# Kernel optimization log

Hardware: AMD Instinct MI355X
Metric: run time of the kernel (lower is better)

Reference implementation:

```python
import jax, jax.numpy as jnp
import numpy as np

B, OBS, H, A = 500000, 128, 64, 16


def setup_inputs() -> dict:
    key = jax.random.key(0)
    ks = jax.random.split(key, 10)
    return {
        "x": jax.random.normal(ks[0], (B, OBS), dtype=jnp.float32),
        "hidden_states": jax.random.normal(ks[1], (B, H), dtype=jnp.float32),
        "active_masks": jax.random.randint(ks[2], (B,), 0, 2, dtype=jnp.int32),
        "fc1_w": jax.random.normal(ks[3], (H, OBS), dtype=jnp.float32) * 0.05,
        "fc1_b": jnp.zeros((H,), dtype=jnp.float32),
        "w_ih": jax.random.normal(ks[4], (3 * H, H), dtype=jnp.float32) * 0.05,
        "w_hh": jax.random.normal(ks[5], (3 * H, H), dtype=jnp.float32) * 0.05,
        "b_ih": jnp.zeros((3 * H,), dtype=jnp.float32),
        "b_hh": jnp.zeros((3 * H,), dtype=jnp.float32),
        "fc2_w": jax.random.normal(ks[6], (A, H), dtype=jnp.float32) * 0.01,
        "fc2_b": jnp.zeros((A,), dtype=jnp.float32),
    }


def reference(x, hidden_states, active_masks, fc1_w, fc1_b, w_ih, w_hh, b_ih, b_hh, fc2_w, fc2_b):
    # fc1 + tanh: [B, H]
    a = jnp.tanh(x @ fc1_w.T + fc1_b)
    # GRUCell (torch convention): gates = [r, z, n]
    gi = a @ w_ih.T + b_ih                      # [B, 3H]
    gh = hidden_states @ w_hh.T + b_hh          # [B, 3H]
    i_r, i_z, i_n = jnp.split(gi, 3, axis=-1)
    h_r, h_z, h_n = jnp.split(gh, 3, axis=-1)
    r = jax.nn.sigmoid(i_r + h_r)
    z = jax.nn.sigmoid(i_z + h_z)
    n = jnp.tanh(i_n + r * h_n)
    h_upd = (1.0 - z) * n + z * hidden_states
    # Selective update: active agents get the GRU step, sleepers keep state.
    mask = (active_masks != 0)[:, None]          # [B, 1]
    new_hidden = jnp.where(mask, h_upd, hidden_states)
    logits = new_hidden @ fc2_w.T + fc2_b        # [B, A]
    return logits, new_hidden
```

## Files before the change

### kernel.cpp

```cpp
#include <hip/hip_runtime.h>


#define BB   500000
#define OBSN 128
#define HD   64
#define ADIM 16
#define NTIL (BB / 16)
#define GRID 512
#define GWAV (GRID * 8)

typedef __attribute__((ext_vector_type(8))) short short8;
typedef __attribute__((ext_vector_type(4))) float f32x4;

__device__ __forceinline__ unsigned short f2b(float f) {
  union { float f; unsigned u; } c; c.f = f;
  return (unsigned short)((c.u + 0x7fffu + ((c.u >> 16) & 1u)) >> 16);
}
__device__ __forceinline__ unsigned pk2(float a, float b) {
  return (unsigned)f2b(a) | ((unsigned)f2b(b) << 16);
}
__device__ __forceinline__ short8 cvt_frag(float4 a, float4 b) {
  union { short8 v; unsigned u[4]; } t;
  t.u[0] = pk2(a.x, a.y); t.u[1] = pk2(a.z, a.w);
  t.u[2] = pk2(b.x, b.y); t.u[3] = pk2(b.z, b.w);
  return t.v;
}
__device__ __forceinline__ float fsigmoid(float x) {
  return __builtin_amdgcn_rcpf(1.f + __builtin_amdgcn_exp2f(-1.44269504f * x));
}
__device__ __forceinline__ float ftanh(float x) {
  return 1.f - 2.f * __builtin_amdgcn_rcpf(1.f + __builtin_amdgcn_exp2f(2.88539008f * x));
}

__global__ void convert_weights(const float* __restrict__ fc1_w,
                                const float* __restrict__ w_ih,
                                const float* __restrict__ w_hh,
                                const float* __restrict__ fc2_w,
                                unsigned short* __restrict__ ws) {
  int i = blockIdx.x * 256 + threadIdx.x;
  if (i < 8192) {
    int n = i >> 7, k = (i & 127) ^ ((n & 7) << 3);
    ws[i] = f2b(fc1_w[n * 128 + k]);
  } else if (i < 24576) {
    int j = i - 8192, n = j >> 7, k = (j & 127) ^ ((n & 7) << 3);
    float v = (k < 64) ? w_ih[n * 64 + k] : w_hh[n * 64 + (k - 64)];
    ws[i] = f2b(v);
  } else if (i < 28672) {
    int j = i - 24576, n = j >> 6, k = (j & 63) ^ ((n & 7) << 3);
    ws[i] = f2b(w_ih[8192 + n * 64 + k]);
  } else if (i < 32768) {
    int j = i - 28672, n = j >> 6, k = (j & 63) ^ ((n & 7) << 3);
    ws[i] = f2b(w_hh[8192 + n * 64 + k]);
  } else if (i < 33792) {
    int j = i - 32768, n = j >> 6, k = (j & 63) ^ ((n & 7) << 3);
    ws[i] = f2b(fc2_w[n * 64 + k]);
  }
}

struct Batch {
  float4 x[8];
  float4 h[4];
  int4   am4;
};

#define LDS_FENCE() asm volatile("s_waitcnt lgkmcnt(0)" ::: "memory")

__global__ __launch_bounds__(512) void gru_actor_main(
    const float* __restrict__ x, const float* __restrict__ hs,
    const int* __restrict__ am,
    const float* __restrict__ fc1_b, const float* __restrict__ b_ih,
    const float* __restrict__ b_hh, const float* __restrict__ fc2_b,
    const unsigned short* __restrict__ wb, float* __restrict__ out) {
  __shared__ __align__(16) unsigned short lw[33792];
  __shared__ __align__(16) unsigned short sb_all[8][16 * 72];
  __shared__ __align__(16) float hf_all[8][16 * 68];

  const int tid = threadIdx.x;
#pragma unroll
  for (int i = 0; i < 9; ++i) {
    int c = tid + i * 512;
    if (c < 4224) ((short8*)lw)[c] = ((const short8*)wb)[c];
  }
  __syncthreads();

  const int wv = tid >> 6, lane = tid & 63;
  const int col = lane & 15, quad = lane >> 4;
  const int sw = (col & 7) << 3;
  unsigned short* sb = sb_all[wv];
  float* hf = hf_all[wv];

  float b1v[4], brv[4], bzv[4], biv[4], bhv[4];
#pragma unroll
  for (int nt = 0; nt < 4; ++nt) {
    int c = nt * 16 + col;
    b1v[nt] = fc1_b[c];
    brv[nt] = b_ih[c] + b_hh[c];
    bzv[nt] = b_ih[64 + c] + b_hh[64 + c];
    biv[nt] = b_ih[128 + c];
    bhv[nt] = b_hh[128 + c];
  }
  const float b2 = fc2_b[col];
  const f32x4 zero4 = {0.f, 0.f, 0.f, 0.f};

  auto prefetch = [&](Batch& b, int t) {
    const int r0 = t * 16;
    const float* xp = x + (r0 + col) * OBSN + quad * 8;
#pragma unroll
    for (int kt = 0; kt < 4; ++kt) {
      b.x[2 * kt]     = *(const float4*)(xp + kt * 32);
      b.x[2 * kt + 1] = *(const float4*)(xp + kt * 32 + 4);
    }
    const float* hp = hs + (r0 + col) * HD + quad * 8;
#pragma unroll
    for (int kt = 0; kt < 2; ++kt) {
      b.h[2 * kt]     = *(const float4*)(hp + kt * 32);
      b.h[2 * kt + 1] = *(const float4*)(hp + kt * 32 + 4);
    }
    b.am4 = *(const int4*)(am + r0 + quad * 4);
  };

  auto process = [&](const Batch& bt, int t) {
    const int r0 = t * 16;
#pragma unroll
    for (int kt = 0; kt < 2; ++kt) {
      *(float4*)(hf + col * 68 + kt * 32 + quad * 8)     = bt.h[2 * kt];
      *(float4*)(hf + col * 68 + kt * 32 + quad * 8 + 4) = bt.h[2 * kt + 1];
    }
    f32x4 accA[4] = {zero4, zero4, zero4, zero4};
#pragma unroll
    for (int kt = 0; kt < 4; ++kt) {
      short8 af = cvt_frag(bt.x[2 * kt], bt.x[2 * kt + 1]);
#pragma unroll
      for (int nt = 0; nt < 4; ++nt) {
        short8 bf = *(const short8*)(lw + (nt * 16 + col) * 128 + ((kt * 32 + quad * 8) ^ sw));
        accA[nt] = __builtin_amdgcn_mfma_f32_16x16x32_bf16(af, bf, accA[nt], 0, 0, 0);
      }
    }
#pragma unroll
    for (int nt = 0; nt < 4; ++nt) {
#pragma unroll
      for (int rg = 0; rg < 4; ++rg) {
        float a = ftanh(accA[nt][rg] + b1v[nt]);
        sb[(quad * 4 + rg) * 72 + nt * 16 + col] = f2b(a);
      }
    }
    LDS_FENCE();
    f32x4 rz[8]  = {zero4, zero4, zero4, zero4, zero4, zero4, zero4, zero4};
    f32x4 gin[4] = {zero4, zero4, zero4, zero4};
    f32x4 ghn[4] = {zero4, zero4, zero4, zero4};
#pragma unroll
    for (int kt = 0; kt < 2; ++kt) {
      short8 af = *(const short8*)(sb + col * 72 + kt * 32 + quad * 8);
#pragma unroll
      for (int nt = 0; nt < 8; ++nt) {
        short8 bf = *(const short8*)(lw + 8192 + (nt * 16 + col) * 128 + ((kt * 32 + quad * 8) ^ sw));
        rz[nt] = __builtin_amdgcn_mfma_f32_16x16x32_bf16(af, bf, rz[nt], 0, 0, 0);
      }
#pragma unroll
      for (int nt = 0; nt < 4; ++nt) {
        short8 bf = *(const short8*)(lw + 24576 + (nt * 16 + col) * 64 + ((kt * 32 + quad * 8) ^ sw));
        gin[nt] = __builtin_amdgcn_mfma_f32_16x16x32_bf16(af, bf, gin[nt], 0, 0, 0);
      }
    }
#pragma unroll
    for (int kt = 0; kt < 2; ++kt) {
      short8 af = cvt_frag(bt.h[2 * kt], bt.h[2 * kt + 1]);
#pragma unroll
      for (int nt = 0; nt < 8; ++nt) {
        short8 bf = *(const short8*)(lw + 8192 + (nt * 16 + col) * 128 + 64 + ((kt * 32 + quad * 8) ^ sw));
        rz[nt] = __builtin_amdgcn_mfma_f32_16x16x32_bf16(af, bf, rz[nt], 0, 0, 0);
      }
#pragma unroll
      for (int nt = 0; nt < 4; ++nt) {
        short8 bf = *(const short8*)(lw + 28672 + (nt * 16 + col) * 64 + ((kt * 32 + quad * 8) ^ sw));
        ghn[nt] = __builtin_amdgcn_mfma_f32_16x16x32_bf16(af, bf, ghn[nt], 0, 0, 0);
      }
    }
    const int rowbase = r0 + quad * 4;
    const int amr[4] = {bt.am4.x, bt.am4.y, bt.am4.z, bt.am4.w};
#pragma unroll
    for (int nt = 0; nt < 4; ++nt) {
#pragma unroll
      for (int rg = 0; rg < 4; ++rg) {
        float r = fsigmoid(rz[nt][rg] + brv[nt]);
        float z = fsigmoid(rz[nt + 4][rg] + bzv[nt]);
        float n = ftanh(gin[nt][rg] + biv[nt] + r * (ghn[nt][rg] + bhv[nt]));
        float hprev = hf[(quad * 4 + rg) * 68 + nt * 16 + col];
        float hu = (1.f - z) * n + z * hprev;
        float hne = (amr[rg] != 0) ? hu : hprev;
        out[(size_t)BB * ADIM + (size_t)(rowbase + rg) * HD + nt * 16 + col] = hne;
        sb[(quad * 4 + rg) * 72 + nt * 16 + col] = f2b(hne);
      }
    }
    LDS_FENCE();
    f32x4 acc2 = zero4;
#pragma unroll
    for (int kt = 0; kt < 2; ++kt) {
      short8 af = *(const short8*)(sb + col * 72 + kt * 32 + quad * 8);
      short8 bf = *(const short8*)(lw + 32768 + col * 64 + ((kt * 32 + quad * 8) ^ sw));
      acc2 = __builtin_amdgcn_mfma_f32_16x16x32_bf16(af, bf, acc2, 0, 0, 0);
    }
#pragma unroll
    for (int rg = 0; rg < 4; ++rg)
      out[(size_t)(rowbase + rg) * ADIM + col] = acc2[rg] + b2;
  };

  int t = blockIdx.x * 8 + wv;
  if (t >= NTIL) return;
  Batch A, B;
  prefetch(A, t);
  for (;;) {
    int tn = t + GWAV;
    prefetch(B, (tn < NTIL) ? tn : t);
    __builtin_amdgcn_sched_barrier(0);
    process(A, t);
    if (tn >= NTIL) break;
    t = tn;
    tn = t + GWAV;
    prefetch(A, (tn < NTIL) ? tn : t);
    __builtin_amdgcn_sched_barrier(0);
    process(B, t);
    if (tn >= NTIL) break;
    t = tn;
  }
}

extern "C" void kernel_launch(void* const* d_in, const int* in_sizes, int n_in,
                              void* d_out, int out_size, void* d_ws, size_t ws_size,
                              hipStream_t stream) {
  const float* x     = (const float*)d_in[0];
  const float* hsp   = (const float*)d_in[1];
  const int*   amp   = (const int*)d_in[2];
  const float* fc1_w = (const float*)d_in[3];
  const float* fc1_b = (const float*)d_in[4];
  const float* w_ih  = (const float*)d_in[5];
  const float* w_hh  = (const float*)d_in[6];
  const float* b_ih  = (const float*)d_in[7];
  const float* b_hh  = (const float*)d_in[8];
  const float* fc2_w = (const float*)d_in[9];
  const float* fc2_b = (const float*)d_in[10];
  unsigned short* wb = (unsigned short*)d_ws;
  float* out = (float*)d_out;

  convert_weights<<<dim3(132), dim3(256), 0, stream>>>(fc1_w, w_ih, w_hh, fc2_w, wb);
  gru_actor_main<<<dim3(GRID), dim3(512), 0, stream>>>(
      x, hsp, amp, fc1_b, b_ih, b_hh, fc2_b, wb, out);
}
```

Measured before the change: 497.7 us.

## Restructure GRU kernel with in-process prefetch, 12 waves/block, coalesced hidden stores

Moves the next-tile prefetch into the middle of processing: x and the mask are fetched after the fc1 MFMAs, and h after the gate MFMAs, so the live-register window is shorter. Blocks change to 768 threads (12 waves) with a 256-block grid, and one float LDS scratch per wave replaces the separate bf16 and fp32 buffers. Biases move from registers to LDS. New-hidden output is now written as contiguous float4 rows read back from LDS instead of scattered scalars. The trade-off is extra LDS traffic and fences, and a different occupancy balance.

```diff
diff --git a/kernel.cpp b/kernel.cpp
--- a/kernel.cpp
+++ b/kernel.cpp
@@ -6,8 +6,9 @@
 #define HD   64
 #define ADIM 16
 #define NTIL (BB / 16)
-#define GRID 512
-#define GWAV (GRID * 8)
+#define GRID 256
+#define WPB  12
+#define NWAVE (GRID * WPB)
 
 typedef __attribute__((ext_vector_type(8))) short short8;
 typedef __attribute__((ext_vector_type(4))) float f32x4;
@@ -59,73 +60,64 @@
 
 struct Batch {
   float4 x[8];
-  float4 h[4];
   int4   am4;
 };
 
 #define LDS_FENCE() asm volatile("s_waitcnt lgkmcnt(0)" ::: "memory")
-
-__global__ __launch_bounds__(512) void gru_actor_main(
+#define CFENCE()    asm volatile("" ::: "memory")
+
+__global__ __launch_bounds__(768, 3) void gru_actor_main(
     const float* __restrict__ x, const float* __restrict__ hs,
     const int* __restrict__ am,
     const float* __restrict__ fc1_b, const float* __restrict__ b_ih,
     const float* __restrict__ b_hh, const float* __restrict__ fc2_b,
     const unsigned short* __restrict__ wb, float* __restrict__ out) {
   __shared__ __align__(16) unsigned short lw[33792];
-  __shared__ __align__(16) unsigned short sb_all[8][16 * 72];
-  __shared__ __align__(16) float hf_all[8][16 * 68];
+  __shared__ __align__(16) float wsb_all[WPB][16 * 68];
+  __shared__ float bias_lds[336];
 
   const int tid = threadIdx.x;
 #pragma unroll
-  for (int i = 0; i < 9; ++i) {
-    int c = tid + i * 512;
+  for (int i = 0; i < 6; ++i) {
+    int c = tid + i * 768;
     if (c < 4224) ((short8*)lw)[c] = ((const short8*)wb)[c];
   }
+  if (tid < 64)       bias_lds[tid] = fc1_b[tid];
+  else if (tid < 128) { int i = tid - 64;  bias_lds[tid] = b_ih[i] + b_hh[i]; }
+  else if (tid < 192) { int i = tid - 128; bias_lds[tid] = b_ih[64 + i] + b_hh[64 + i]; }
+  else if (tid < 256) { int i = tid - 192; bias_lds[tid] = b_ih[128 + i]; }
+  else if (tid < 320) { int i = tid - 256; bias_lds[tid] = b_hh[128 + i]; }
+  else if (tid < 336) bias_lds[tid] = fc2_b[tid - 320];
   __syncthreads();
 
   const int wv = tid >> 6, lane = tid & 63;
   const int col = lane & 15, quad = lane >> 4;
   const int sw = (col & 7) << 3;
-  unsigned short* sb = sb_all[wv];
-  float* hf = hf_all[wv];
-
-  float b1v[4], brv[4], bzv[4], biv[4], bhv[4];
-#pragma unroll
-  for (int nt = 0; nt < 4; ++nt) {
-    int c = nt * 16 + col;
-    b1v[nt] = fc1_b[c];
-    brv[nt] = b_ih[c] + b_hh[c];
-    bzv[nt] = b_ih[64 + c] + b_hh[64 + c];
-    biv[nt] = b_ih[128 + c];
-    bhv[nt] = b_hh[128 + c];
-  }
-  const float b2 = fc2_b[col];
+  float* wsb = wsb_all[wv];
   const f32x4 zero4 = {0.f, 0.f, 0.f, 0.f};
 
-  auto prefetch = [&](Batch& b, int t) {
-    const int r0 = t * 16;
-    const float* xp = x + (r0 + col) * OBSN + quad * 8;
+  auto pf_xam = [&](Batch& b, int t) {
+    const float* xp = x + (size_t)(t * 16 + col) * OBSN + quad * 8;
 #pragma unroll
     for (int kt = 0; kt < 4; ++kt) {
       b.x[2 * kt]     = *(const float4*)(xp + kt * 32);
       b.x[2 * kt + 1] = *(const float4*)(xp + kt * 32 + 4);
     }
-    const float* hp = hs + (r0 + col) * HD + quad * 8;
-#pragma unroll
-    for (int kt = 0; kt < 2; ++kt) {
-      b.h[2 * kt]     = *(const float4*)(hp + kt * 32);
-      b.h[2 * kt + 1] = *(const float4*)(hp + kt * 32 + 4);
-    }
-    b.am4 = *(const int4*)(am + r0 + quad * 4);
+    b.am4 = *(const int4*)(am + t * 16 + quad * 4);
   };
-
-  auto process = [&](const Batch& bt, int t) {
-    const int r0 = t * 16;
-#pragma unroll
-    for (int kt = 0; kt < 2; ++kt) {
-      *(float4*)(hf + col * 68 + kt * 32 + quad * 8)     = bt.h[2 * kt];
-      *(float4*)(hf + col * 68 + kt * 32 + quad * 8 + 4) = bt.h[2 * kt + 1];
-    }
+  auto pf_h = [&](float4* h, int t) {
+    const float* hp = hs + (size_t)(t * 16 + col) * HD + quad * 8;
+#pragma unroll
+    for (int kt = 0; kt < 2; ++kt) {
+      h[2 * kt]     = *(const float4*)(hp + kt * 32);
+      h[2 * kt + 1] = *(const float4*)(hp + kt * 32 + 4);
+    }
+  };
+
+  auto process = [&](const Batch& bt, const float4* hcur, int t,
+                     Batch& bnxt, float4* hnxt, int tnext) {
+    const int ampk = (bt.am4.x != 0) | ((bt.am4.y != 0) << 1) |
+                     ((bt.am4.z != 0) << 2) | ((bt.am4.w != 0) << 3);
     f32x4 accA[4] = {zero4, zero4, zero4, zero4};
 #pragma unroll
     for (int kt = 0; kt < 4; ++kt) {
@@ -136,21 +128,28 @@
         accA[nt] = __builtin_amdgcn_mfma_f32_16x16x32_bf16(af, bf, accA[nt], 0, 0, 0);
       }
     }
+    pf_xam(bnxt, tnext);
+    __builtin_amdgcn_sched_barrier(0);
 #pragma unroll
     for (int nt = 0; nt < 4; ++nt) {
-#pragma unroll
-      for (int rg = 0; rg < 4; ++rg) {
-        float a = ftanh(accA[nt][rg] + b1v[nt]);
-        sb[(quad * 4 + rg) * 72 + nt * 16 + col] = f2b(a);
-      }
+      float b1 = bias_lds[nt * 16 + col];
+#pragma unroll
+      for (int rg = 0; rg < 4; ++rg)
+        wsb[(quad * 4 + rg) * 68 + nt * 16 + col] = ftanh(accA[nt][rg] + b1);
     }
     LDS_FENCE();
     f32x4 rz[8]  = {zero4, zero4, zero4, zero4, zero4, zero4, zero4, zero4};
     f32x4 gin[4] = {zero4, zero4, zero4, zero4};
     f32x4 ghn[4] = {zero4, zero4, zero4, zero4};
-#pragma unroll
-    for (int kt = 0; kt < 2; ++kt) {
-      short8 af = *(const short8*)(sb + col * 72 + kt * 32 + quad * 8);
+    float4 alo0 = *(const float4*)(wsb + col * 68 + quad * 8);
+    float4 ahi0 = *(const float4*)(wsb + col * 68 + quad * 8 + 4);
+    float4 alo1 = *(const float4*)(wsb + col * 68 + 32 + quad * 8);
+    float4 ahi1 = *(const float4*)(wsb + col * 68 + 32 + quad * 8 + 4);
+    short8 afa0 = cvt_frag(alo0, ahi0);
+    short8 afa1 = cvt_frag(alo1, ahi1);
+#pragma unroll
+    for (int kt = 0; kt < 2; ++kt) {
+      short8 af = kt ? afa1 : afa0;
 #pragma unroll
       for (int nt = 0; nt < 8; ++nt) {
         short8 bf = *(const short8*)(lw + 8192 + (nt * 16 + col) * 128 + ((kt * 32 + quad * 8) ^ sw));
@@ -164,7 +163,7 @@
     }
 #pragma unroll
     for (int kt = 0; kt < 2; ++kt) {
-      short8 af = cvt_frag(bt.h[2 * kt], bt.h[2 * kt + 1]);
+      short8 af = cvt_frag(hcur[2 * kt], hcur[2 * kt + 1]);
 #pragma unroll
       for (int nt = 0; nt < 8; ++nt) {
         short8 bf = *(const short8*)(lw + 8192 + (nt * 16 + col) * 128 + 64 + ((kt * 32 + quad * 8) ^ sw));
@@ -176,50 +175,69 @@
         ghn[nt] = __builtin_amdgcn_mfma_f32_16x16x32_bf16(af, bf, ghn[nt], 0, 0, 0);
       }
     }
-    const int rowbase = r0 + quad * 4;
-    const int amr[4] = {bt.am4.x, bt.am4.y, bt.am4.z, bt.am4.w};
+    CFENCE();
+#pragma unroll
+    for (int kt = 0; kt < 2; ++kt) {
+      *(float4*)(wsb + col * 68 + kt * 32 + quad * 8)     = hcur[2 * kt];
+      *(float4*)(wsb + col * 68 + kt * 32 + quad * 8 + 4) = hcur[2 * kt + 1];
+    }
+    pf_h(hnxt, tnext);
+    __builtin_amdgcn_sched_barrier(0);
+    LDS_FENCE();
 #pragma unroll
     for (int nt = 0; nt < 4; ++nt) {
+      int c = nt * 16 + col;
+      float br = bias_lds[64 + c], bz = bias_lds[128 + c];
+      float bi = bias_lds[192 + c], bh = bias_lds[256 + c];
 #pragma unroll
       for (int rg = 0; rg < 4; ++rg) {
-        float r = fsigmoid(rz[nt][rg] + brv[nt]);
-        float z = fsigmoid(rz[nt + 4][rg] + bzv[nt]);
-        float n = ftanh(gin[nt][rg] + biv[nt] + r * (ghn[nt][rg] + bhv[nt]));
-        float hprev = hf[(quad * 4 + rg) * 68 + nt * 16 + col];
+        float r = fsigmoid(rz[nt][rg] + br);
+        float z = fsigmoid(rz[nt + 4][rg] + bz);
+        float n = ftanh(gin[nt][rg] + bi + r * (ghn[nt][rg] + bh));
+        float hprev = wsb[(quad * 4 + rg) * 68 + c];
         float hu = (1.f - z) * n + z * hprev;
-        float hne = (amr[rg] != 0) ? hu : hprev;
-        out[(size_t)BB * ADIM + (size_t)(rowbase + rg) * HD + nt * 16 + col] = hne;
-        sb[(quad * 4 + rg) * 72 + nt * 16 + col] = f2b(hne);
+        wsb[(quad * 4 + rg) * 68 + c] = ((ampk >> rg) & 1) ? hu : hprev;
       }
     }
     LDS_FENCE();
+    float4 rlo0 = *(const float4*)(wsb + col * 68 + quad * 8);
+    float4 rhi0 = *(const float4*)(wsb + col * 68 + quad * 8 + 4);
+    float4 rlo1 = *(const float4*)(wsb + col * 68 + 32 + quad * 8);
+    float4 rhi1 = *(const float4*)(wsb + col * 68 + 32 + quad * 8 + 4);
+    float* op = out + (size_t)BB * ADIM + (size_t)(t * 16 + col) * HD + quad * 8;
+    *(float4*)(op)          = rlo0;
+    *(float4*)(op + 4)      = rhi0;
+    *(float4*)(op + 32)     = rlo1;
+    *(float4*)(op + 32 + 4) = rhi1;
     f32x4 acc2 = zero4;
-#pragma unroll
-    for (int kt = 0; kt < 2; ++kt) {
-      short8 af = *(const short8*)(sb + col * 72 + kt * 32 + quad * 8);
-      short8 bf = *(const short8*)(lw + 32768 + col * 64 + ((kt * 32 + quad * 8) ^ sw));
-      acc2 = __builtin_amdgcn_mfma_f32_16x16x32_bf16(af, bf, acc2, 0, 0, 0);
-    }
+    {
+      short8 af0 = cvt_frag(rlo0, rhi0);
+      short8 bf0 = *(const short8*)(lw + 32768 + col * 64 + ((quad * 8) ^ sw));
+      acc2 = __builtin_amdgcn_mfma_f32_16x16x32_bf16(af0, bf0, acc2, 0, 0, 0);
+      short8 af1 = cvt_frag(rlo1, rhi1);
+      short8 bf1 = *(const short8*)(lw + 32768 + col * 64 + ((32 + quad * 8) ^ sw));
+      acc2 = __builtin_amdgcn_mfma_f32_16x16x32_bf16(af1, bf1, acc2, 0, 0, 0);
+    }
+    float b2 = bias_lds[320 + col];
 #pragma unroll
     for (int rg = 0; rg < 4; ++rg)
-      out[(size_t)(rowbase + rg) * ADIM + col] = acc2[rg] + b2;
+      out[(size_t)(t * 16 + quad * 4 + rg) * ADIM + col] = acc2[rg] + b2;
   };
 
-  int t = blockIdx.x * 8 + wv;
-  if (t >= NTIL) return;
+  int t = blockIdx.x * WPB + wv;
   Batch A, B;
-  prefetch(A, t);
+  float4 hA[4], hB[4];
+  pf_xam(A, t);
+  pf_h(hA, t);
   for (;;) {
-    int tn = t + GWAV;
-    prefetch(B, (tn < NTIL) ? tn : t);
-    __builtin_amdgcn_sched_barrier(0);
-    process(A, t);
+    int tn = t + NWAVE;
+    int ts = (tn < NTIL) ? tn : t;
+    process(A, hA, t, B, hB, ts);
     if (tn >= NTIL) break;
     t = tn;
-    tn = t + GWAV;
-    prefetch(A, (tn < NTIL) ? tn : t);
-    __builtin_amdgcn_sched_barrier(0);
-    process(B, t);
+    tn = t + NWAVE;
+    ts = (tn < NTIL) ? tn : t;
+    process(B, hB, t, A, hA, ts);
     if (tn >= NTIL) break;
     t = tn;
   }
@@ -243,6 +261,6 @@
   float* out = (float*)d_out;
 
   convert_weights<<<dim3(132), dim3(256), 0, stream>>>(fc1_w, w_ih, w_hh, fc2_w, wb);
-  gru_actor_main<<<dim3(GRID), dim3(512), 0, stream>>>(
+  gru_actor_main<<<dim3(GRID), dim3(768), 0, stream>>>(
       x, hsp, amp, fc1_b, b_ih, b_hh, fc2_b, wb, out);
 }
```

After: 498.7 us. No clear change (+0.2%).
